# Kernel optimization log

Measured on AMD Instinct MI355X. Metric: run time of the kernel, lower is better.

The kernel has to match this reference:

```python
import jax, jax.numpy as jnp
import numpy as np

N = 50000
F_IN = 128
HID = 16
CLS = 40
NEG_SLOPE = 0.2


def gat_layer(x, src, dst, W, a_src, a_dst, b, heads, out_ch):
    # x: [N, Fin]; src/dst: [E] (self-loops included); W: [Fin, heads*out_ch]
    n = x.shape[0]
    h = (x @ W).reshape(n, heads, out_ch)                    # [N, H, C]
    al_s = jnp.einsum('nhc,hc->nh', h, a_src)                # [N, H]
    al_d = jnp.einsum('nhc,hc->nh', h, a_dst)                # [N, H]
    e = jax.nn.leaky_relu(al_s[src] + al_d[dst], NEG_SLOPE)  # [E, H]
    # segment softmax over incoming edges of each dst node
    m = jax.ops.segment_max(e, dst, num_segments=n)          # [N, H]
    ex = jnp.exp(e - m[dst])
    den = jax.ops.segment_sum(ex, dst, num_segments=n)
    alpha = ex / den[dst]                                    # [E, H]
    out = jax.ops.segment_sum(h[src] * alpha[:, :, None], dst, num_segments=n)
    return out.reshape(n, heads * out_ch) + b


def setup_inputs() -> dict:
    key = jax.random.key(0)
    ks = jax.random.split(key, 16)
    E = 800000
    x = jax.random.normal(ks[0], (N, F_IN), dtype=jnp.float32)
    edge_index = jax.random.randint(ks[1], (2, E), 0, N, dtype=jnp.int64)
    s = 0.1
    W1 = jax.random.normal(ks[2], (F_IN, 7 * HID), dtype=jnp.float32) * s
    a_src1 = jax.random.normal(ks[3], (7, HID), dtype=jnp.float32) * s
    a_dst1 = jax.random.normal(ks[4], (7, HID), dtype=jnp.float32) * s
    b1 = jnp.zeros((7 * HID,), dtype=jnp.float32)
    W2 = jax.random.normal(ks[5], (7 * HID, 6 * HID), dtype=jnp.float32) * s
    a_src2 = jax.random.normal(ks[6], (6, HID), dtype=jnp.float32) * s
    a_dst2 = jax.random.normal(ks[7], (6, HID), dtype=jnp.float32) * s
    b2 = jnp.zeros((6 * HID,), dtype=jnp.float32)
    W3 = jax.random.normal(ks[8], (6 * HID, 6 * CLS), dtype=jnp.float32) * s
    a_src3 = jax.random.normal(ks[9], (6, CLS), dtype=jnp.float32) * s
    a_dst3 = jax.random.normal(ks[10], (6, CLS), dtype=jnp.float32) * s
    b3 = jnp.zeros((6 * CLS,), dtype=jnp.float32)
    return {
        'x': x, 'edge_index': edge_index,
        'W1': W1, 'a_src1': a_src1, 'a_dst1': a_dst1, 'b1': b1,
        'W2': W2, 'a_src2': a_src2, 'a_dst2': a_dst2, 'b2': b2,
        'W3': W3, 'a_src3': a_src3, 'a_dst3': a_dst3, 'b3': b3,
    }


def reference(x, edge_index, W1, a_src1, a_dst1, b1, W2, a_src2, a_dst2, b2, W3, a_src3, a_dst3, b3):
    # add self-loops once (PyG GATConv default add_self_loops=True)
    loops = jnp.arange(N, dtype=edge_index.dtype)
    src = jnp.concatenate([edge_index[0], loops])
    dst = jnp.concatenate([edge_index[1], loops])
    # dropout layers are identity in eval mode
    h = gat_layer(x, src, dst, W1, a_src1, a_dst1, b1, 7, HID)
    h = jax.nn.relu(h)
    h = gat_layer(h, src, dst, W2, a_src2, a_dst2, b2, 6, HID)
    h = jax.nn.relu(h)
    out = gat_layer(h, src, dst, W3, a_src3, a_dst3, b3, 6, CLS)
    return out
```

## Files before the change

### kernel.cpp

```cpp
#include <hip/hip_runtime.h>
#include <hip/hip_fp16.h>
#include <cstdint>

#define NNODES 50000

__device__ inline void wave_lds_fence() {
  asm volatile("s_waitcnt lgkmcnt(0)" ::: "memory");
  __builtin_amdgcn_wave_barrier();
}

__global__ void hist_kernel(const int* __restrict__ ei, int E, int Nn, int* __restrict__ cnt) {
  int i = blockIdx.x * blockDim.x + threadIdx.x;
  int ET = E + Nn;
  if (i >= ET) return;
  int d = (i < E) ? ei[E + i] : (i - E);
  atomicAdd(&cnt[d], 1);
}

__global__ void scan1_kernel(const int* __restrict__ in, int n, int* __restrict__ incl,
                             int* __restrict__ bsum) {
  __shared__ int sd[256];
  int g = blockIdx.x * 256 + threadIdx.x;
  int v = (g < n) ? in[g] : 0;
  sd[threadIdx.x] = v;
  __syncthreads();
  for (int off = 1; off < 256; off <<= 1) {
    int t = (threadIdx.x >= off) ? sd[threadIdx.x - off] : 0;
    __syncthreads();
    sd[threadIdx.x] += t;
    __syncthreads();
  }
  if (g < n) incl[g] = sd[threadIdx.x];
  if (threadIdx.x == 255) bsum[blockIdx.x] = sd[255];
}

__global__ void scan3_kernel(const int* __restrict__ incl, const int* __restrict__ bscan,
                             int n, int* __restrict__ rowptr) {
  int g = blockIdx.x * 256 + threadIdx.x;
  if (g == 0) rowptr[0] = 0;
  if (g < n) {
    int off = (blockIdx.x > 0) ? bscan[blockIdx.x - 1] : 0;
    rowptr[g + 1] = incl[g] + off;
  }
}

__global__ void scatter_kernel(const int* __restrict__ ei, int E, int Nn,
                               const int* __restrict__ rowptr, int* __restrict__ cnt2,
                               int* __restrict__ esorted) {
  int i = blockIdx.x * blockDim.x + threadIdx.x;
  int ET = E + Nn;
  if (i >= ET) return;
  int s, d;
  if (i < E) { s = ei[i]; d = ei[E + i]; }
  else       { s = i - E; d = i - E; }
  int pos = rowptr[d] + atomicAdd(&cnt2[d], 1);
  esorted[pos] = s;
}

template <int FIN, int H, int C, int HCP, int BLOCK>
__global__ __launch_bounds__(BLOCK) void gemm_alpha_kernel(const float* __restrict__ X,
                                                           const float* __restrict__ W,
                                                           const float* __restrict__ a_s,
                                                           const float* __restrict__ a_d,
                                                           __half* __restrict__ Hout,
                                                           float* __restrict__ als8,
                                                           float* __restrict__ ald8) {
  constexpr int HC = H * C;
  constexpr int NT = 16;
  constexpr int TM = 4, TN = 4;
  constexpr int CG = HC / TN;
  __shared__ __align__(16) float xs[FIN * NT];
  __shared__ float red[NT][8][2];
  const int n0 = blockIdx.x * NT;
  for (int i = threadIdx.x * 4; i < NT * FIN; i += BLOCK * 4) {
    float4 v = *(const float4*)(X + (size_t)n0 * FIN + i);
    int node = i / FIN, k = i % FIN;
    xs[(k + 0) * NT + node] = v.x;
    xs[(k + 1) * NT + node] = v.y;
    xs[(k + 2) * NT + node] = v.z;
    xs[(k + 3) * NT + node] = v.w;
  }
  for (int z = threadIdx.x; z < NT * 8 * 2; z += BLOCK) ((float*)red)[z] = 0.f;
  __syncthreads();
  const int cg = threadIdx.x % CG;
  const int ng = threadIdx.x / CG;
  const bool compute = (ng < NT / TM);
  const int c0 = cg * TN;
  const int i0 = ng * TM;
  float acc[TM][TN];
#pragma unroll
  for (int i = 0; i < TM; ++i)
#pragma unroll
    for (int j = 0; j < TN; ++j) acc[i][j] = 0.f;
  if (compute) {
#pragma unroll 4
    for (int k = 0; k < FIN; ++k) {
      const float4 wv = *(const float4*)(W + (size_t)k * HC + c0);
      const float4 xv = *(const float4*)(xs + k * NT + i0);
      acc[0][0] += xv.x * wv.x; acc[0][1] += xv.x * wv.y; acc[0][2] += xv.x * wv.z; acc[0][3] += xv.x * wv.w;
      acc[1][0] += xv.y * wv.x; acc[1][1] += xv.y * wv.y; acc[1][2] += xv.y * wv.z; acc[1][3] += xv.y * wv.w;
      acc[2][0] += xv.z * wv.x; acc[2][1] += xv.z * wv.y; acc[2][2] += xv.z * wv.z; acc[2][3] += xv.z * wv.w;
      acc[3][0] += xv.w * wv.x; acc[3][1] += xv.w * wv.y; acc[3][2] += xv.w * wv.z; acc[3][3] += xv.w * wv.w;
    }
#pragma unroll
    for (int i = 0; i < TM; ++i) {
      union { __half2 h2[2]; uint2 u; } pk;
      pk.h2[0] = __floats2half2_rn(acc[i][0], acc[i][1]);
      pk.h2[1] = __floats2half2_rn(acc[i][2], acc[i][3]);
      *(uint2*)(Hout + (size_t)(n0 + i0 + i) * HCP + c0) = pk.u;
    }
    const int hd = c0 / C;
    const float4 as4 = *(const float4*)(a_s + c0);
    const float4 ad4 = *(const float4*)(a_d + c0);
#pragma unroll
    for (int i = 0; i < TM; ++i) {
      float ps = acc[i][0] * as4.x + acc[i][1] * as4.y + acc[i][2] * as4.z + acc[i][3] * as4.w;
      float pd = acc[i][0] * ad4.x + acc[i][1] * ad4.y + acc[i][2] * ad4.z + acc[i][3] * ad4.w;
      atomicAdd(&red[i0 + i][hd][0], ps);
      atomicAdd(&red[i0 + i][hd][1], pd);
    }
  }
  __syncthreads();
  for (int z = threadIdx.x; z < NT * H; z += BLOCK) {
    int n = z / H, h = z % H;
    als8[(size_t)(n0 + n) * 8 + h] = red[n][h][0];
    ald8[(size_t)(n0 + n) * 8 + h] = red[n][h][1];
  }
}

template <int H, int C, int HCP, int RELU>
__global__ __launch_bounds__(256) void agg_kernel(const __half* __restrict__ Hbuf,
                                                  const float* __restrict__ als8,
                                                  const float* __restrict__ ald8,
                                                  const int* __restrict__ rowptr,
                                                  const int* __restrict__ esrc,
                                                  const float* __restrict__ bias,
                                                  float* __restrict__ Out, int n_nodes) {
  constexpr int HC = H * C;
  constexpr int NCHUNK = HC / 8;
  constexpr int GROUPS = (NCHUNK <= 16) ? 4 : 2;
  constexpr int LPG = 64 / GROUPS;
  constexpr int UN = 3;
  constexpr int TPAD = 72;
  const int wave = threadIdx.x >> 6;
  const int lane = threadIdx.x & 63;
  const int grp = lane / LPG;
  const int lg = lane % LPG;
  const int n = blockIdx.x * 4 + wave;
  __shared__ float s_w[4][TPAD * H];
  __shared__ int s_src[4][TPAD];
  if (n >= n_nodes) return;

  if (lane < TPAD - 64) s_src[wave][64 + lane] = 0;
  for (int z = lane; z < (TPAD - 64) * H; z += 64) s_w[wave][64 * H + z] = 0.f;

  const int e0 = rowptr[n];
  const int e1 = rowptr[n + 1];

  float aldn[H];
#pragma unroll
  for (int h = 0; h < H; ++h) aldn[h] = ald8[n * 8 + h];

  const int head = min((lg * 8) / C, H - 1);
  const bool act = lg < NCHUNK;

  float acc[8];
  float lsum = 0.f;
#pragma unroll
  for (int j = 0; j < 8; ++j) acc[j] = 0.f;

  for (int base = e0; base < e1; base += 64) {
    const int cnt = (e1 - base < 64) ? (e1 - base) : 64;
    int sreg = 0;
    if (lane < cnt) sreg = esrc[base + lane];
    s_src[wave][lane] = sreg;
    if (lane < cnt) {
      const float4 qa = *(const float4*)(als8 + (size_t)sreg * 8);
      const float4 qb = *(const float4*)(als8 + (size_t)sreg * 8 + 4);
      const float q[8] = {qa.x, qa.y, qa.z, qa.w, qb.x, qb.y, qb.z, qb.w};
#pragma unroll
      for (int h = 0; h < H; ++h) {
        float v = q[h] + aldn[h];
        v = v > 0.f ? v : 0.2f * v;
        s_w[wave][lane * H + h] = __expf(v);
      }
    } else {
#pragma unroll
      for (int h = 0; h < H; ++h) s_w[wave][lane * H + h] = 0.f;
    }
    wave_lds_fence();
    const int nit = (cnt + GROUPS - 1) / GROUPS;
    for (int i = 0; i < nit; i += UN) {
      int tt[UN], si[UN];
      uint4 v[UN];
      float w[UN];
#pragma unroll
      for (int k = 0; k < UN; ++k) tt[k] = (i + k) * GROUPS + grp;
#pragma unroll
      for (int k = 0; k < UN; ++k) si[k] = s_src[wave][tt[k]];
#pragma unroll
      for (int k = 0; k < UN; ++k)
        if (act) v[k] = *(const uint4*)(Hbuf + (size_t)si[k] * HCP + lg * 8);
#pragma unroll
      for (int k = 0; k < UN; ++k) w[k] = s_w[wave][tt[k] * H + head];
#pragma unroll
      for (int k = 0; k < UN; ++k)
        if (act) {
          const __half2* hp = (const __half2*)&v[k];
          float2 f0 = __half22float2(hp[0]);
          float2 f1 = __half22float2(hp[1]);
          float2 f2 = __half22float2(hp[2]);
          float2 f3 = __half22float2(hp[3]);
          lsum += w[k];
          acc[0] += w[k] * f0.x; acc[1] += w[k] * f0.y;
          acc[2] += w[k] * f1.x; acc[3] += w[k] * f1.y;
          acc[4] += w[k] * f2.x; acc[5] += w[k] * f2.y;
          acc[6] += w[k] * f3.x; acc[7] += w[k] * f3.y;
        }
    }
    wave_lds_fence();
  }

#pragma unroll
  for (int off = LPG; off < 64; off <<= 1) {
    lsum += __shfl_xor(lsum, off);
#pragma unroll
    for (int j = 0; j < 8; ++j) acc[j] += __shfl_xor(acc[j], off);
  }

  if (grp == 0 && act) {
    const float inv = 1.f / lsum;
    const float4 b0 = *(const float4*)(bias + 2 * lg * 4);
    const float4 b1 = *(const float4*)(bias + 2 * lg * 4 + 4);
    float4 o0, o1;
    o0.x = acc[0] * inv + b0.x; o0.y = acc[1] * inv + b0.y;
    o0.z = acc[2] * inv + b0.z; o0.w = acc[3] * inv + b0.w;
    o1.x = acc[4] * inv + b1.x; o1.y = acc[5] * inv + b1.y;
    o1.z = acc[6] * inv + b1.z; o1.w = acc[7] * inv + b1.w;
    if (RELU) {
      o0.x = fmaxf(o0.x, 0.f); o0.y = fmaxf(o0.y, 0.f);
      o0.z = fmaxf(o0.z, 0.f); o0.w = fmaxf(o0.w, 0.f);
      o1.x = fmaxf(o1.x, 0.f); o1.y = fmaxf(o1.y, 0.f);
      o1.z = fmaxf(o1.z, 0.f); o1.w = fmaxf(o1.w, 0.f);
    }
    *(float4*)(Out + (size_t)n * HC + lg * 8) = o0;
    *(float4*)(Out + (size_t)n * HC + lg * 8 + 4) = o1;
  }
}

extern "C" void kernel_launch(void* const* d_in, const int* in_sizes, int n_in,
                              void* d_out, int out_size, void* d_ws, size_t ws_size,
                              hipStream_t stream) {
  const int N = NNODES;
  const float* x  = (const float*)d_in[0];
  const int* ei   = (const int*)d_in[1];
  const float* W1 = (const float*)d_in[2];
  const float* as1 = (const float*)d_in[3];
  const float* ad1 = (const float*)d_in[4];
  const float* b1  = (const float*)d_in[5];
  const float* W2  = (const float*)d_in[6];
  const float* as2 = (const float*)d_in[7];
  const float* ad2 = (const float*)d_in[8];
  const float* b2  = (const float*)d_in[9];
  const float* W3  = (const float*)d_in[10];
  const float* as3 = (const float*)d_in[11];
  const float* ad3 = (const float*)d_in[12];
  const float* b3  = (const float*)d_in[13];
  float* out = (float*)d_out;
  const int E = in_sizes[1] / 2;
  const int ET = E + N;

  char* ws = (char*)d_ws;
  size_t off = 0;
  auto alloc = [&](size_t bytes) -> char* {
    char* p = ws + off;
    off += (bytes + 255) & ~(size_t)255;
    return p;
  };
  int* cnt     = (int*)alloc((size_t)N * 4);
  int* cnt2    = (int*)alloc((size_t)N * 4);
  int* incl    = (int*)alloc((size_t)N * 4);
  int* bsum    = (int*)alloc(512 * 4);
  int* bscan   = (int*)alloc(256 * 4);
  int* rowptr  = (int*)alloc((size_t)(N + 1) * 4);
  int* esorted = (int*)alloc((size_t)ET * 4);
  float* als   = (float*)alloc((size_t)N * 8 * 4);
  float* ald   = (float*)alloc((size_t)N * 8 * 4);
  __half* hbuf = (__half*)alloc((size_t)N * 256 * 2);
  float* abuf  = (float*)alloc((size_t)N * 112 * 4);

  hipMemsetAsync(cnt, 0, (size_t)N * 4, stream);
  hipMemsetAsync(cnt2, 0, (size_t)N * 4, stream);

  const int B1 = (N + 255) / 256;
  hist_kernel<<<(ET + 255) / 256, 256, 0, stream>>>(ei, E, N, cnt);
  scan1_kernel<<<B1, 256, 0, stream>>>(cnt, N, incl, bsum);
  scan1_kernel<<<1, 256, 0, stream>>>(bsum, B1, bscan, bsum + 256);
  scan3_kernel<<<B1, 256, 0, stream>>>(incl, bscan, N, rowptr);
  scatter_kernel<<<(ET + 255) / 256, 256, 0, stream>>>(ei, E, N, rowptr, cnt2, esorted);

  gemm_alpha_kernel<128, 7, 16, 128, 128><<<N / 16, 128, 0, stream>>>(x, W1, as1, ad1, hbuf, als, ald);
  agg_kernel<7, 16, 128, 1><<<(N + 3) / 4, 256, 0, stream>>>(hbuf, als, ald, rowptr, esorted, b1, abuf, N);
  gemm_alpha_kernel<112, 6, 16, 96, 128><<<N / 16, 128, 0, stream>>>(abuf, W2, as2, ad2, hbuf, als, ald);
  agg_kernel<6, 16, 96, 1><<<(N + 3) / 4, 256, 0, stream>>>(hbuf, als, ald, rowptr, esorted, b2, abuf, N);
  gemm_alpha_kernel<96, 6, 40, 256, 256><<<N / 16, 256, 0, stream>>>(abuf, W3, as3, ad3, hbuf, als, ald);
  agg_kernel<6, 40, 256, 0><<<(N + 3) / 4, 256, 0, stream>>>(hbuf, als, ald, rowptr, esorted, b3, out, N);
}
```

Baseline: 519.1 us.

## Rewrite node-feature GEMM with fp16 MFMA and shuffle-based attention reductions

Replaces the scalar fp32 register-tiled GEMM with a 64-node-tile kernel that stages X and W as fp16 in LDS and computes with 16x16x32 f16 MFMA instructions. The attention logits are reduced with intra-wave shuffles per 16-column tile instead of LDS atomics, with handling for tiles that span two heads. W columns are processed in groups of up to 8 tiles with reloads. This trades fp32 input precision for matrix-core throughput and adds boundary handling for a partial last tile.

```diff
diff --git a/kernel.cpp b/kernel.cpp
--- a/kernel.cpp
+++ b/kernel.cpp
@@ -3,6 +3,10 @@
 #include <cstdint>
 
 #define NNODES 50000
+
+typedef _Float16 f16x8 __attribute__((ext_vector_type(8)));
+typedef _Float16 f16x4 __attribute__((ext_vector_type(4)));
+typedef float f32x4 __attribute__((ext_vector_type(4)));
 
 __device__ inline void wave_lds_fence() {
   asm volatile("s_waitcnt lgkmcnt(0)" ::: "memory");
@@ -57,74 +61,128 @@
   esorted[pos] = s;
 }
 
-template <int FIN, int H, int C, int HCP, int BLOCK>
-__global__ __launch_bounds__(BLOCK) void gemm_alpha_kernel(const float* __restrict__ X,
-                                                           const float* __restrict__ W,
-                                                           const float* __restrict__ a_s,
-                                                           const float* __restrict__ a_d,
-                                                           __half* __restrict__ Hout,
-                                                           float* __restrict__ als8,
-                                                           float* __restrict__ ald8) {
+template <int FIN, int H, int C, int HCP>
+__global__ __launch_bounds__(256) void gemm_alpha_kernel(const float* __restrict__ X,
+                                                         const float* __restrict__ W,
+                                                         const float* __restrict__ a_s,
+                                                         const float* __restrict__ a_d,
+                                                         __half* __restrict__ Hout,
+                                                         float* __restrict__ als8,
+                                                         float* __restrict__ ald8,
+                                                         int n_nodes) {
   constexpr int HC = H * C;
-  constexpr int NT = 16;
-  constexpr int TM = 4, TN = 4;
-  constexpr int CG = HC / TN;
-  __shared__ __align__(16) float xs[FIN * NT];
-  __shared__ float red[NT][8][2];
+  constexpr int NT = 64;
+  constexpr int KS = (FIN + 31) / 32;
+  constexpr int KPAD = KS * 32;
+  constexpr int KP = KPAD + 8;
+  constexpr int TILES = HC / 16;
+  constexpr int TG = (TILES < 8) ? TILES : 8;
+  constexpr int BLOCK = 256;
+  __shared__ __align__(16) _Float16 xls[NT][KP];
+  __shared__ __align__(16) _Float16 wt[TG * 16][KP];
+  __shared__ float redS[NT][TILES][2];
+  __shared__ float redD[NT][TILES][2];
+  const int tid = threadIdx.x;
   const int n0 = blockIdx.x * NT;
-  for (int i = threadIdx.x * 4; i < NT * FIN; i += BLOCK * 4) {
-    float4 v = *(const float4*)(X + (size_t)n0 * FIN + i);
-    int node = i / FIN, k = i % FIN;
-    xs[(k + 0) * NT + node] = v.x;
-    xs[(k + 1) * NT + node] = v.y;
-    xs[(k + 2) * NT + node] = v.z;
-    xs[(k + 3) * NT + node] = v.w;
-  }
-  for (int z = threadIdx.x; z < NT * 8 * 2; z += BLOCK) ((float*)red)[z] = 0.f;
+  const int nv = min(n_nodes - n0, NT);
+
+  for (int i = tid * 4; i < NT * KPAD; i += BLOCK * 4) {
+    int node = i / KPAD, k = i % KPAD;
+    float4 v = make_float4(0.f, 0.f, 0.f, 0.f);
+    if (node < nv && k < FIN) v = *(const float4*)(X + (size_t)(n0 + node) * FIN + k);
+    f16x4 h;
+    h[0] = (_Float16)v.x; h[1] = (_Float16)v.y; h[2] = (_Float16)v.z; h[3] = (_Float16)v.w;
+    *(f16x4*)(&xls[node][k]) = h;
+  }
+  {
+    const int cw = ((TILES < TG ? TILES : TG)) * 16;
+    for (int i = tid * 4; i < KPAD * cw; i += BLOCK * 4) {
+      int k = i / cw, c = i % cw;
+      float4 v = make_float4(0.f, 0.f, 0.f, 0.f);
+      if (k < FIN) v = *(const float4*)(W + (size_t)k * HC + c);
+      wt[c + 0][k] = (_Float16)v.x; wt[c + 1][k] = (_Float16)v.y;
+      wt[c + 2][k] = (_Float16)v.z; wt[c + 3][k] = (_Float16)v.w;
+    }
+  }
   __syncthreads();
-  const int cg = threadIdx.x % CG;
-  const int ng = threadIdx.x / CG;
-  const bool compute = (ng < NT / TM);
-  const int c0 = cg * TN;
-  const int i0 = ng * TM;
-  float acc[TM][TN];
-#pragma unroll
-  for (int i = 0; i < TM; ++i)
-#pragma unroll
-    for (int j = 0; j < TN; ++j) acc[i][j] = 0.f;
-  if (compute) {
-#pragma unroll 4
-    for (int k = 0; k < FIN; ++k) {
-      const float4 wv = *(const float4*)(W + (size_t)k * HC + c0);
-      const float4 xv = *(const float4*)(xs + k * NT + i0);
-      acc[0][0] += xv.x * wv.x; acc[0][1] += xv.x * wv.y; acc[0][2] += xv.x * wv.z; acc[0][3] += xv.x * wv.w;
-      acc[1][0] += xv.y * wv.x; acc[1][1] += xv.y * wv.y; acc[1][2] += xv.y * wv.z; acc[1][3] += xv.y * wv.w;
-      acc[2][0] += xv.z * wv.x; acc[2][1] += xv.z * wv.y; acc[2][2] += xv.z * wv.z; acc[2][3] += xv.z * wv.w;
-      acc[3][0] += xv.w * wv.x; acc[3][1] += xv.w * wv.y; acc[3][2] += xv.w * wv.z; acc[3][3] += xv.w * wv.w;
-    }
-#pragma unroll
-    for (int i = 0; i < TM; ++i) {
-      union { __half2 h2[2]; uint2 u; } pk;
-      pk.h2[0] = __floats2half2_rn(acc[i][0], acc[i][1]);
-      pk.h2[1] = __floats2half2_rn(acc[i][2], acc[i][3]);
-      *(uint2*)(Hout + (size_t)(n0 + i0 + i) * HCP + c0) = pk.u;
-    }
-    const int hd = c0 / C;
-    const float4 as4 = *(const float4*)(a_s + c0);
-    const float4 ad4 = *(const float4*)(a_d + c0);
-#pragma unroll
-    for (int i = 0; i < TM; ++i) {
-      float ps = acc[i][0] * as4.x + acc[i][1] * as4.y + acc[i][2] * as4.z + acc[i][3] * as4.w;
-      float pd = acc[i][0] * ad4.x + acc[i][1] * ad4.y + acc[i][2] * ad4.z + acc[i][3] * ad4.w;
-      atomicAdd(&red[i0 + i][hd][0], ps);
-      atomicAdd(&red[i0 + i][hd][1], pd);
-    }
-  }
+
+  const int wid = tid >> 6;
+  const int l = tid & 63;
+  const int l15 = l & 15;
+  const int g = l >> 4;
+  const int nodeBase = wid * 16;
+
+  f16x8 afr[KS];
+#pragma unroll
+  for (int ks = 0; ks < KS; ++ks)
+    afr[ks] = *(const f16x8*)(&xls[nodeBase + l15][32 * ks + 8 * g]);
+
+  int cbase = 0;
+  while (true) {
+    const int tc = (TILES - cbase < TG) ? (TILES - cbase) : TG;
+#pragma unroll 1
+    for (int t = 0; t < tc; ++t) {
+      const int ct = cbase + t;
+      f32x4 acc = {0.f, 0.f, 0.f, 0.f};
+#pragma unroll
+      for (int ks = 0; ks < KS; ++ks) {
+        f16x8 b = *(const f16x8*)(&wt[16 * t + l15][32 * ks + 8 * g]);
+        acc = __builtin_amdgcn_mfma_f32_16x16x32_f16(afr[ks], b, acc, 0, 0, 0);
+      }
+      const int colg = 16 * ct + l15;
+      const int lo = (16 * ct) / C;
+      const bool mixed = (lo != (16 * ct + 15) / C);
+      const float as_c = a_s[colg], ad_c = a_d[colg];
+      const float inlo = ((colg / C) == lo) ? 1.f : 0.f;
+#pragma unroll
+      for (int q = 0; q < 4; ++q) {
+        const int r = 4 * g + q;
+        if (nodeBase + r < nv)
+          Hout[(size_t)(n0 + nodeBase + r) * HCP + colg] = __float2half(acc[q]);
+        float pts = acc[q] * as_c, ptd = acc[q] * ad_c;
+        float p0s = pts * inlo, p0d = ptd * inlo;
+#pragma unroll
+        for (int o = 1; o < 16; o <<= 1) {
+          pts += __shfl_xor(pts, o);
+          ptd += __shfl_xor(ptd, o);
+          if (mixed) { p0s += __shfl_xor(p0s, o); p0d += __shfl_xor(p0d, o); }
+        }
+        if (!mixed) { p0s = pts; p0d = ptd; }
+        if (l15 == 0) {
+          redS[nodeBase + r][ct][0] = p0s; redS[nodeBase + r][ct][1] = pts - p0s;
+          redD[nodeBase + r][ct][0] = p0d; redD[nodeBase + r][ct][1] = ptd - p0d;
+        }
+      }
+    }
+    cbase += tc;
+    if (cbase >= TILES) break;
+    __syncthreads();
+    const int cw = ((TILES - cbase < TG) ? (TILES - cbase) : TG) * 16;
+    const int c0g = cbase * 16;
+    for (int i = tid * 4; i < KPAD * cw; i += BLOCK * 4) {
+      int k = i / cw, c = i % cw;
+      float4 v = make_float4(0.f, 0.f, 0.f, 0.f);
+      if (k < FIN) v = *(const float4*)(W + (size_t)k * HC + c0g + c);
+      wt[c + 0][k] = (_Float16)v.x; wt[c + 1][k] = (_Float16)v.y;
+      wt[c + 2][k] = (_Float16)v.z; wt[c + 3][k] = (_Float16)v.w;
+    }
+    __syncthreads();
+  }
+
   __syncthreads();
-  for (int z = threadIdx.x; z < NT * H; z += BLOCK) {
+  for (int z = tid; z < NT * H; z += BLOCK) {
     int n = z / H, h = z % H;
-    als8[(size_t)(n0 + n) * 8 + h] = red[n][h][0];
-    ald8[(size_t)(n0 + n) * 8 + h] = red[n][h][1];
+    if (n < nv) {
+      float ss = 0.f, dd = 0.f;
+#pragma unroll
+      for (int ct = 0; ct < TILES; ++ct) {
+        int lo = (16 * ct) / C;
+        if (lo == h)          { ss += redS[n][ct][0]; dd += redD[n][ct][0]; }
+        else if (lo + 1 == h) { ss += redS[n][ct][1]; dd += redD[n][ct][1]; }
+      }
+      als8[(size_t)(n0 + n) * 8 + h] = ss;
+      ald8[(size_t)(n0 + n) * 8 + h] = dd;
+    }
   }
 }
 
@@ -230,8 +288,8 @@
 
   if (grp == 0 && act) {
     const float inv = 1.f / lsum;
-    const float4 b0 = *(const float4*)(bias + 2 * lg * 4);
-    const float4 b1 = *(const float4*)(bias + 2 * lg * 4 + 4);
+    const float4 b0 = *(const float4*)(bias + lg * 8);
+    const float4 b1 = *(const float4*)(bias + lg * 8 + 4);
     float4 o0, o1;
     o0.x = acc[0] * inv + b0.x; o0.y = acc[1] * inv + b0.y;
     o0.z = acc[2] * inv + b0.z; o0.w = acc[3] * inv + b0.w;
@@ -299,10 +357,12 @@
   scan3_kernel<<<B1, 256, 0, stream>>>(incl, bscan, N, rowptr);
   scatter_kernel<<<(ET + 255) / 256, 256, 0, stream>>>(ei, E, N, rowptr, cnt2, esorted);
 
-  gemm_alpha_kernel<128, 7, 16, 128, 128><<<N / 16, 128, 0, stream>>>(x, W1, as1, ad1, hbuf, als, ald);
+  const int GB = (N + 63) / 64;
+
+  gemm_alpha_kernel<128, 7, 16, 128><<<GB, 256, 0, stream>>>(x, W1, as1, ad1, hbuf, als, ald, N);
   agg_kernel<7, 16, 128, 1><<<(N + 3) / 4, 256, 0, stream>>>(hbuf, als, ald, rowptr, esorted, b1, abuf, N);
-  gemm_alpha_kernel<112, 6, 16, 96, 128><<<N / 16, 128, 0, stream>>>(abuf, W2, as2, ad2, hbuf, als, ald);
+  gemm_alpha_kernel<112, 6, 16, 96><<<GB, 256, 0, stream>>>(abuf, W2, as2, ad2, hbuf, als, ald, N);
   agg_kernel<6, 16, 96, 1><<<(N + 3) / 4, 256, 0, stream>>>(hbuf, als, ald, rowptr, esorted, b2, abuf, N);
-  gemm_alpha_kernel<96, 6, 40, 256, 256><<<N / 16, 256, 0, stream>>>(abuf, W3, as3, ad3, hbuf, als, ald);
+  gemm_alpha_kernel<96, 6, 40, 256><<<GB, 256, 0, stream>>>(abuf, W3, as3, ad3, hbuf, als, ald, N);
   agg_kernel<6, 40, 256, 0><<<(N + 3) / 4, 256, 0, stream>>>(hbuf, als, ald, rowptr, esorted, b3, out, N);
 }
```

Result: faster. 493.2 us (-5.0%).
